# Kernel optimization log

Hardware: AMD Instinct MI355X
Metric: run time of the kernel (lower is better)

Reference implementation:

```python
import jax, jax.numpy as jnp
import numpy as np

B, NQ, D, H, L, P, FFN = 32, 300, 256, 8, 3, 4, 1024
SPATIAL = [(80, 80), (40, 40), (20, 20)]  # static multi-scale feature shapes (640px, strides 8/16/32)
S = sum(h * w for h, w in SPATIAL)  # 8400
HD = D // H


def _ln(x, g, b, eps=1e-5):
    m = jnp.mean(x, -1, keepdims=True)
    v = jnp.mean((x - m) ** 2, -1, keepdims=True)
    return (x - m) * jax.lax.rsqrt(v + eps) * g + b


def _grid_sample(img, grid):
    # img: (N,C,Hh,Ww); grid: (N,Q,Pp,2) in [-1,1]; bilinear, zeros padding, align_corners=False
    N, C, Hh, Ww = img.shape
    x = (grid[..., 0] + 1.0) * (Ww * 0.5) - 0.5
    y = (grid[..., 1] + 1.0) * (Hh * 0.5) - 0.5
    x0 = jnp.floor(x)
    y0 = jnp.floor(y)
    wx1 = x - x0
    wy1 = y - y0
    x0i = x0.astype(jnp.int32)
    y0i = y0.astype(jnp.int32)
    flat = img.reshape(N, C, Hh * Ww)
    Q, Pp = grid.shape[1], grid.shape[2]

    def corner(xi, yi, w):
        valid = (xi >= 0) & (xi < Ww) & (yi >= 0) & (yi < Hh)
        idx = jnp.clip(yi, 0, Hh - 1) * Ww + jnp.clip(xi, 0, Ww - 1)
        v = jnp.take_along_axis(flat, idx.reshape(N, 1, Q * Pp), axis=2).reshape(N, C, Q, Pp)
        return v * (w * valid)[:, None]

    return (corner(x0i, y0i, (1 - wx1) * (1 - wy1))
            + corner(x0i + 1, y0i, wx1 * (1 - wy1))
            + corner(x0i, y0i + 1, (1 - wx1) * wy1)
            + corner(x0i + 1, y0i + 1, wx1 * wy1))


def setup_inputs() -> dict:
    key = jax.random.key(0)
    ks = iter(jax.random.split(key, 32))
    inp = {
        'hidden_states': jax.random.normal(next(ks), (B, NQ, D), jnp.float32),
        'position_embeddings': jax.random.normal(next(ks), (B, NQ, D), jnp.float32),
        'reference_points': jax.random.uniform(next(ks), (B, NQ, 1, 4), jnp.float32, 0.1, 0.9),
        'encoder_hidden_states': jax.random.normal(next(ks), (B, S, D), jnp.float32),
    }
    for name, shape in [('Wq', (D, D)), ('Wk', (D, D)), ('Wv', (D, D)), ('Wo', (D, D)),
                        ('Woff', (D, H * L * P * 2)), ('Waw', (D, H * L * P)),
                        ('Wval', (D, D)), ('Wout', (D, D)), ('W1', (D, FFN)), ('W2', (FFN, D))]:
        inp[name] = jax.random.normal(next(ks), shape, jnp.float32) * 0.02
    for name, dim in [('bq', D), ('bk', D), ('bv', D), ('bo', D), ('boff', H * L * P * 2),
                      ('baw', H * L * P), ('bval', D), ('bout', D), ('b1', FFN), ('b2', D)]:
        inp[name] = jnp.zeros((dim,), jnp.float32)
    for g, bname in [('ln1_g', 'ln1_b'), ('ln2_g', 'ln2_b'), ('ln3_g', 'ln3_b')]:
        inp[g] = jnp.ones((D,), jnp.float32)
        inp[bname] = jnp.zeros((D,), jnp.float32)
    return inp


def reference(hidden_states, position_embeddings, reference_points, encoder_hidden_states,
              Wq, bq, Wk, bk, Wv, bv, Wo, bo, ln1_g, ln1_b,
              Woff, boff, Waw, baw, Wval, bval, Wout, bout, ln2_g, ln2_b,
              W1, b1, W2, b2, ln3_g, ln3_b):
    hs = hidden_states
    # ---- self attention (pos-embedded q/k, raw v) ----
    hp = hs + position_embeddings
    q = ((hp @ Wq + bq) * (HD ** -0.5)).reshape(B, NQ, H, HD)
    k = (hp @ Wk + bk).reshape(B, NQ, H, HD)
    v = (hs @ Wv + bv).reshape(B, NQ, H, HD)
    attn = jax.nn.softmax(jnp.einsum('bqhd,bkhd->bhqk', q, k), axis=-1)
    sa = jnp.einsum('bhqk,bkhd->bqhd', attn, v).reshape(B, NQ, D) @ Wo + bo
    hs = _ln(hs + sa, ln1_g, ln1_b)
    # ---- multi-scale deformable cross attention ----
    hp = hs + position_embeddings
    value = (encoder_hidden_states @ Wval + bval).reshape(B, S, H, HD)
    off = (hp @ Woff + boff).reshape(B, NQ, H, L, P, 2)
    aw = jax.nn.softmax((hp @ Waw + baw).reshape(B, NQ, H, L * P), axis=-1).reshape(B, NQ, H, L, P)
    ref = reference_points  # (B,NQ,1,4) boxes -> 4-coord branch
    loc = ref[:, :, None, :, None, :2] + off / P * ref[:, :, None, :, None, 2:] * 0.5
    grids = (2.0 * loc - 1.0).transpose(0, 2, 1, 3, 4, 5).reshape(B * H, NQ, L, P, 2)
    start = 0
    samples = []
    for lvl, (hh, ww) in enumerate(SPATIAL):
        v_l = value[:, start:start + hh * ww]  # (B,hw,H,HD)
        start += hh * ww
        v_l = v_l.transpose(0, 2, 3, 1).reshape(B * H, HD, hh, ww)
        samples.append(_grid_sample(v_l, grids[:, :, lvl]))  # (B*H,HD,NQ,P)
    sampled = jnp.stack(samples, axis=3).reshape(B * H, HD, NQ, L * P)
    w = aw.transpose(0, 2, 1, 3, 4).reshape(B * H, 1, NQ, L * P)
    ca = (sampled * w).sum(-1).reshape(B, H * HD, NQ).transpose(0, 2, 1) @ Wout + bout
    hs = _ln(hs + ca, ln2_g, ln2_b)
    # ---- FFN ----
    ff = jax.nn.relu(hs @ W1 + b1) @ W2 + b2
    return _ln(hs + ff, ln3_g, ln3_b)
```

## Files before the change

kernel.cpp:

```cpp
#include <hip/hip_runtime.h>
#include <hip/hip_bf16.h>

typedef unsigned int  uint32;
typedef unsigned short ushort16;
typedef __bf16 bfx8 __attribute__((ext_vector_type(8)));
typedef float  f32x4 __attribute__((ext_vector_type(4)));

typedef __attribute__((address_space(1))) const unsigned int gas_u32;
typedef __attribute__((address_space(3))) unsigned int las_u32;

#define B_   32
#define NQ_  300
#define D_   256
#define H_   8
#define HD_  32
#define L_   3
#define P_   4
#define S_   8400
#define FFN_ 1024
#define M1   (B_*NQ_)
#define MV   (B_*S_)
#define NQP  320
#define NQT  19

__device__ inline ushort16 f2bf(float x) {
  uint32 u = __float_as_uint(x);
  uint32 r = u + 0x7fffu + ((u >> 16) & 1u);
  return (ushort16)(r >> 16);
}
__device__ inline float bf2f(ushort16 v) {
  return __uint_as_float(((uint32)v) << 16);
}
__device__ inline uint32 cvtpk(float lo, float hi) {
  uint32 r; asm("v_cvt_pk_bf16_f32 %0, %1, %2" : "=v"(r) : "v"(lo), "v"(hi)); return r;
}

__global__ __launch_bounds__(256) void rt_add(const float* __restrict__ a,
                                              const float* __restrict__ b,
                                              float* __restrict__ o, int n4)
{
  int i = blockIdx.x * 256 + threadIdx.x;
  if (i < n4) {
    float4 x = ((const float4*)a)[i];
    float4 y = ((const float4*)b)[i];
    float4 z; z.x = x.x + y.x; z.y = x.y + y.y; z.z = x.z + y.z; z.w = x.w + y.w;
    ((float4*)o)[i] = z;
  }
}

__global__ __launch_bounds__(256) void rt_wt(const float* __restrict__ W,
                                             ushort16* __restrict__ WT,
                                             int K, int N, int Npad)
{
  __shared__ float t[32][33];
  int n0 = blockIdx.x * 32, k0 = blockIdx.y * 32;
  int c = threadIdx.x & 31, r = threadIdx.x >> 5;
#pragma unroll
  for (int i = 0; i < 4; i++) {
    int kk = k0 + r + i * 8;
    int nn = n0 + c;
    t[r + i * 8][c] = (nn < N) ? W[(size_t)kk * N + nn] : 0.f;
  }
  __syncthreads();
#pragma unroll
  for (int i = 0; i < 4; i++) {
    int nn = n0 + r + i * 8;
    int kk = k0 + c;
    if (nn < Npad) WT[(size_t)nn * K + kk] = f2bf(t[c][r + i * 8]);
  }
}

__global__ __launch_bounds__(256) void rt_wc(const float* __restrict__ W,
                                             ushort16* __restrict__ WC)
{
  int gid = blockIdx.x * 256 + threadIdx.x;
  int c = gid >> 8, n = gid & 255;
  uint4 u;
  uint32 w0 = (uint32)f2bf(W[(c*8+0)*256 + n]) | ((uint32)f2bf(W[(c*8+1)*256 + n]) << 16);
  uint32 w1 = (uint32)f2bf(W[(c*8+2)*256 + n]) | ((uint32)f2bf(W[(c*8+3)*256 + n]) << 16);
  uint32 w2 = (uint32)f2bf(W[(c*8+4)*256 + n]) | ((uint32)f2bf(W[(c*8+5)*256 + n]) << 16);
  uint32 w3 = (uint32)f2bf(W[(c*8+6)*256 + n]) | ((uint32)f2bf(W[(c*8+7)*256 + n]) << 16);
  u.x = w0; u.y = w1; u.z = w2; u.w = w3;
  *(uint4*)&WC[(size_t)c * 2048 + n * 8] = u;
}

__global__ __launch_bounds__(1024, 1) void rt_vgemm(
    const float* __restrict__ A, const ushort16* __restrict__ BC,
    const float* __restrict__ bias, ushort16* __restrict__ Vout)
{
  __shared__ __align__(16) char ldsB[131072];
  const int tid = threadIdx.x;
  const int lane = tid & 63, w = tid >> 6;
  const int l15 = lane & 15, l4 = lane >> 4;
  const int bm = blockIdx.x * 256;
  const int arow = bm + w * 16 + l15;
  const float* Ap = A + (size_t)arow * 256 + l4 * 8;

#pragma unroll
  for (int i = 0; i < 8; ++i)
    __builtin_amdgcn_global_load_lds(
        (gas_u32*)(const void*)((const char*)BC + tid * 16 + i * 16384),
        (las_u32*)(void*)(&ldsB[tid * 16 + i * 16384]), 16, 0, 0);

  f32x4 aA = *(const f32x4*)(Ap +  0);
  f32x4 aB = *(const f32x4*)(Ap +  4);
  f32x4 aC = *(const f32x4*)(Ap + 32);
  f32x4 aD = *(const f32x4*)(Ap + 36);

  f32x4 acc[16];
#pragma unroll
  for (int i = 0; i < 16; ++i) acc[i] = (f32x4){0.f, 0.f, 0.f, 0.f};

  __syncthreads();

#pragma unroll
  for (int tt = 0; tt < 4; ++tt) {
    {
      const int t = 2 * tt;
      uint4 u;
      u.x = cvtpk(aA[0], aA[1]); u.y = cvtpk(aA[2], aA[3]);
      u.z = cvtpk(aB[0], aB[1]); u.w = cvtpk(aB[2], aB[3]);
      bfx8 af = __builtin_bit_cast(bfx8, u);
      if (tt < 3) {
        aA = *(const f32x4*)(Ap + (t + 2) * 32);
        aB = *(const f32x4*)(Ap + (t + 2) * 32 + 4);
      }
      const char* bp = &ldsB[(t * 4 + l4) * 4096 + l15 * 16];
#pragma unroll
      for (int ni = 0; ni < 16; ++ni) {
        bfx8 bg = *(const bfx8*)(const void*)(bp + ni * 256);
        acc[ni] = __builtin_amdgcn_mfma_f32_16x16x32_bf16(af, bg, acc[ni], 0, 0, 0);
      }
    }
    {
      const int t = 2 * tt + 1;
      uint4 u;
      u.x = cvtpk(aC[0], aC[1]); u.y = cvtpk(aC[2], aC[3]);
      u.z = cvtpk(aD[0], aD[1]); u.w = cvtpk(aD[2], aD[3]);
      bfx8 af = __builtin_bit_cast(bfx8, u);
      if (tt < 3) {
        aC = *(const f32x4*)(Ap + (t + 2) * 32);
        aD = *(const f32x4*)(Ap + (t + 2) * 32 + 4);
      }
      const char* bp = &ldsB[(t * 4 + l4) * 4096 + l15 * 16];
#pragma unroll
      for (int ni = 0; ni < 16; ++ni) {
        bfx8 bg = *(const bfx8*)(const void*)(bp + ni * 256);
        acc[ni] = __builtin_amdgcn_mfma_f32_16x16x32_bf16(af, bg, acc[ni], 0, 0, 0);
      }
    }
  }

  const int orow = bm + w * 16 + l4 * 4;
#pragma unroll
  for (int ni = 0; ni < 16; ++ni) {
    int col = ni * 16 + l15;
    float bv = bias[col];
    int hh = col >> 5, hd = col & 31;
#pragma unroll
    for (int r = 0; r < 4; ++r) {
      int row = orow + r;
      int bb = row / S_, s = row - bb * S_;
      Vout[(((size_t)bb * H_ + hh) * S_ + s) * HD_ + hd] = f2bf(acc[ni][r] + bv);
    }
  }
}

#define GBM 128
#define GBN 128
#define GBK 32
#define LDP 40

__global__ __launch_bounds__(256) void rt_mgemm(
    const float* __restrict__ A, const ushort16* __restrict__ BT,
    const float* __restrict__ bias, float* __restrict__ C,
    ushort16* __restrict__ Sc,
    int M, int N, int K, float scale, int mode)
{
  __shared__ __align__(16) ushort16 As[GBM][LDP];
  __shared__ __align__(16) ushort16 Bs[GBN][LDP];
  const int tid  = threadIdx.x;
  const int lane = tid & 63;
  const int w    = tid >> 6;
  const int wr   = (w >> 1) * 64;
  const int wc   = (w & 1) * 64;
  const int bm   = blockIdx.y * GBM;
  const int bn   = blockIdx.x * GBN;
  const int l15  = lane & 15;
  const int l4   = lane >> 4;

  f32x4 acc[4][4];
#pragma unroll
  for (int i = 0; i < 4; i++)
#pragma unroll
    for (int j = 0; j < 4; j++)
      acc[i][j] = (f32x4){0.f, 0.f, 0.f, 0.f};

  const int arow = tid >> 3, akc = tid & 7;
  const int brow = tid >> 2, bkc = tid & 3;

  for (int k0 = 0; k0 < K; k0 += GBK) {
#pragma unroll
    for (int i = 0; i < 4; i++) {
      int row = arow + i * 32;
      f32x4 v = *(const f32x4*)(A + (size_t)(bm + row) * K + k0 + akc * 4);
      uint2 u;
      u.x = (uint32)f2bf(v.x) | ((uint32)f2bf(v.y) << 16);
      u.y = (uint32)f2bf(v.z) | ((uint32)f2bf(v.w) << 16);
      *(uint2*)(&As[row][akc * 4]) = u;
    }
#pragma unroll
    for (int i = 0; i < 2; i++) {
      int row = brow + i * 64;
      uint4 v = *(const uint4*)(BT + (size_t)(bn + row) * K + k0 + bkc * 8);
      *(uint4*)(&Bs[row][bkc * 8]) = v;
    }
    __syncthreads();

    bfx8 af[4], bg[4];
#pragma unroll
    for (int mi = 0; mi < 4; mi++)
      af[mi] = *(const bfx8*)(&As[wr + mi * 16 + l15][l4 * 8]);
#pragma unroll
    for (int ni = 0; ni < 4; ni++)
      bg[ni] = *(const bfx8*)(&Bs[wc + ni * 16 + l15][l4 * 8]);
#pragma unroll
    for (int mi = 0; mi < 4; mi++)
#pragma unroll
      for (int ni = 0; ni < 4; ni++)
        acc[mi][ni] = __builtin_amdgcn_mfma_f32_16x16x32_bf16(af[mi], bg[ni], acc[mi][ni], 0, 0, 0);
    __syncthreads();
  }

#pragma unroll
  for (int mi = 0; mi < 4; mi++) {
#pragma unroll
    for (int ni = 0; ni < 4; ni++) {
      int col = bn + wc + ni * 16 + l15;
      if (col >= N) continue;
      float bv = bias[col];
#pragma unroll
      for (int r = 0; r < 4; r++) {
        int row = bm + wr + mi * 16 + l4 * 4 + r;
        float vv = (acc[mi][ni][r] + bv) * scale;
        if (mode == 1) vv = fmaxf(vv, 0.f);
        if (mode == 2) {
          int bb = row / S_, s = row - bb * S_;
          int hh = col >> 5, hd = col & 31;
          Sc[(((size_t)bb * H_ + hh) * S_ + s) * HD_ + hd] = f2bf(vv);
        } else if (mode == 3) {
          int bb = row / NQ_, q = row - bb * NQ_;
          int hh = col >> 5, hd = col & 31;
          Sc[(((size_t)bb * H_ + hh) * NQP + q) * HD_ + hd] = f2bf(vv);
        } else {
          C[(size_t)row * N + col] = vv;
        }
      }
    }
  }
}

__global__ __launch_bounds__(256) void rt_vtr(const ushort16* __restrict__ vh,
                                              ushort16* __restrict__ vt)
{
  __shared__ ushort16 t[64][33];
  int bh = blockIdx.x;
  const ushort16* src = vh + (size_t)bh * NQP * HD_;
  ushort16* dst = vt + (size_t)bh * HD_ * NQP;
  int tid = threadIdx.x;
  int lrow = tid >> 2, lc8 = (tid & 3) * 8;
  int ohd = tid >> 3, oq8 = (tid & 7) * 8;
  for (int r0 = 0; r0 < NQP; r0 += 64) {
    uint4 v = *(const uint4*)(src + (size_t)(r0 + lrow) * HD_ + lc8);
    ushort16* tp = &t[lrow][lc8];
    tp[0] = (ushort16)(v.x & 0xffff); tp[1] = (ushort16)(v.x >> 16);
    tp[2] = (ushort16)(v.y & 0xffff); tp[3] = (ushort16)(v.y >> 16);
    tp[4] = (ushort16)(v.z & 0xffff); tp[5] = (ushort16)(v.z >> 16);
    tp[6] = (ushort16)(v.w & 0xffff); tp[7] = (ushort16)(v.w >> 16);
    __syncthreads();
    uint4 o;
    o.x = (uint32)t[oq8 + 0][ohd] | ((uint32)t[oq8 + 1][ohd] << 16);
    o.y = (uint32)t[oq8 + 2][ohd] | ((uint32)t[oq8 + 3][ohd] << 16);
    o.z = (uint32)t[oq8 + 4][ohd] | ((uint32)t[oq8 + 5][ohd] << 16);
    o.w = (uint32)t[oq8 + 6][ohd] | ((uint32)t[oq8 + 7][ohd] << 16);
    *(uint4*)(dst + (size_t)ohd * NQP + r0 + oq8) = o;
    __syncthreads();
  }
}

__global__ __launch_bounds__(256) void rt_fattn(
    const ushort16* __restrict__ qh, const ushort16* __restrict__ kh,
    const ushort16* __restrict__ vt, float* __restrict__ O)
{
  int gw  = blockIdx.x * 4 + (threadIdx.x >> 6);
  int bh  = gw / NQT, qt = gw - bh * NQT;
  int b   = bh >> 3, h = bh & 7;
  int lane = threadIdx.x & 63;
  int l15 = lane & 15, l4 = lane >> 4;
  int kb4 = l4 * 4;
  const ushort16* Qb = qh + (size_t)bh * NQP * HD_;
  const ushort16* Kb = kh + (size_t)bh * NQP * HD_;
  const ushort16* Vb = vt + (size_t)bh * HD_ * NQP;
  int q = qt * 16 + l15;

  bfx8 bgQ = *(const bfx8*)(const void*)(Qb + (size_t)q * HD_ + l4 * 8);
  f32x4 o0 = {0.f,0.f,0.f,0.f}, o1 = {0.f,0.f,0.f,0.f};
  float m = -1e30f, ssum = 0.f;

  for (int k0 = 0; k0 < NQP; k0 += 32) {
    bfx8 afk0 = *(const bfx8*)(const void*)(Kb + (size_t)(k0 + l15) * HD_ + l4 * 8);
    bfx8 afk1 = *(const bfx8*)(const void*)(Kb + (size_t)(k0 + 16 + l15) * HD_ + l4 * 8);
    f32x4 z = {0.f,0.f,0.f,0.f};
    f32x4 s0 = __builtin_amdgcn_mfma_f32_16x16x32_bf16(afk0, bgQ, z, 0, 0, 0);
    f32x4 s1 = __builtin_amdgcn_mfma_f32_16x16x32_bf16(afk1, bgQ, z, 0, 0, 0);
    int ka = k0 + kb4, kbb = k0 + 16 + kb4;
#pragma unroll
    for (int r = 0; r < 4; r++) {
      if (ka  + r >= NQ_) s0[r] = -1e30f;
      if (kbb + r >= NQ_) s1[r] = -1e30f;
    }
    float cm = fmaxf(fmaxf(fmaxf(s0[0], s0[1]), fmaxf(s0[2], s0[3])),
                     fmaxf(fmaxf(s1[0], s1[1]), fmaxf(s1[2], s1[3])));
    cm = fmaxf(cm, __shfl_xor(cm, 16));
    cm = fmaxf(cm, __shfl_xor(cm, 32));
    float nm = fmaxf(m, cm);
    float sc = __expf(m - nm);
    m = nm;
    f32x4 p0, p1;
#pragma unroll
    for (int r = 0; r < 4; r++) { p0[r] = __expf(s0[r] - m); p1[r] = __expf(s1[r] - m); }
    float ls = (p0[0]+p0[1]+p0[2]+p0[3]) + (p1[0]+p1[1]+p1[2]+p1[3]);
    ls += __shfl_xor(ls, 16);
    ls += __shfl_xor(ls, 32);
    ssum = ssum * sc + ls;

    uint32 t0w0 = cvtpk(p0[0], p0[1]);
    uint32 t0w1 = cvtpk(p0[2], p0[3]);
    uint32 t1w0 = cvtpk(p1[0], p1[1]);
    uint32 t1w1 = cvtpk(p1[2], p1[3]);
    int srcA = l15 + 32 * (l4 & 1);
    int srcB = srcA + 16;
    uint32 a00 = __shfl((int)t0w0, srcA), a01 = __shfl((int)t0w1, srcA);
    uint32 b00 = __shfl((int)t0w0, srcB), b01 = __shfl((int)t0w1, srcB);
    uint32 a10 = __shfl((int)t1w0, srcA), a11 = __shfl((int)t1w1, srcA);
    uint32 b10 = __shfl((int)t1w0, srcB), b11 = __shfl((int)t1w1, srcB);
    bool hi = (l4 >= 2);
    uint4 pw;
    pw.x = hi ? a10 : a00;
    pw.y = hi ? a11 : a01;
    pw.z = hi ? b10 : b00;
    pw.w = hi ? b11 : b01;
    bfx8 bgP = __builtin_bit_cast(bfx8, pw);

    bfx8 afv0 = *(const bfx8*)(const void*)(Vb + (size_t)l15 * NQP + k0 + l4 * 8);
    bfx8 afv1 = *(const bfx8*)(const void*)(Vb + (size_t)(16 + l15) * NQP + k0 + l4 * 8);
#pragma unroll
    for (int r = 0; r < 4; r++) { o0[r] *= sc; o1[r] *= sc; }
    o0 = __builtin_amdgcn_mfma_f32_16x16x32_bf16(afv0, bgP, o0, 0, 0, 0);
    o1 = __builtin_amdgcn_mfma_f32_16x16x32_bf16(afv1, bgP, o1, 0, 0, 0);
  }

  if (q < NQ_) {
    float inv = 1.f / ssum;
    float* op = O + ((size_t)(b * NQ_ + q)) * D_ + h * HD_ + kb4;
    f32x4 r0, r1;
#pragma unroll
    for (int r = 0; r < 4; r++) { r0[r] = o0[r] * inv; r1[r] = o1[r] * inv; }
    *(f32x4*)op = r0;
    *(f32x4*)(op + 16) = r1;
  }
}

__global__ __launch_bounds__(256) void rt_ln(
    const float* __restrict__ X, const float* __restrict__ R,
    const float* __restrict__ g, const float* __restrict__ be,
    float* __restrict__ O, int rows)
{
  int row = blockIdx.x * 4 + (threadIdx.x >> 6);
  int lane = threadIdx.x & 63;
  if (row >= rows) return;
  size_t base = (size_t)row * D_ + lane * 4;
  float4 x = *(const float4*)(X + base);
  float4 r = *(const float4*)(R + base);
  float v0 = x.x + r.x, v1 = x.y + r.y, v2 = x.z + r.z, v3 = x.w + r.w;
  float s = v0 + v1 + v2 + v3;
  float sq = v0*v0 + v1*v1 + v2*v2 + v3*v3;
#pragma unroll
  for (int o = 32; o >= 1; o >>= 1) { s += __shfl_xor(s, o); sq += __shfl_xor(sq, o); }
  float mean = s * (1.f / D_);
  float var  = sq * (1.f / D_) - mean * mean;
  float inv  = 1.f / sqrtf(var + 1e-5f);
  int c = lane * 4;
  float4 gv = *(const float4*)(g + c);
  float4 bv = *(const float4*)(be + c);
  float4 o4;
  o4.x = (v0 - mean) * inv * gv.x + bv.x;
  o4.y = (v1 - mean) * inv * gv.y + bv.y;
  o4.z = (v2 - mean) * inv * gv.z + bv.z;
  o4.w = (v3 - mean) * inv * gv.w + bv.w;
  *(float4*)(O + base) = o4;
}

__global__ __launch_bounds__(256) void rt_awsm(float* __restrict__ aw, int groups)
{
  int gidx = blockIdx.x * 256 + threadIdx.x;
  if (gidx >= groups) return;
  float* p = aw + (size_t)gidx * 12;
  float e[12]; float m = -1e30f;
#pragma unroll
  for (int i = 0; i < 12; i++) { e[i] = p[i]; m = fmaxf(m, e[i]); }
  float s = 0.f;
#pragma unroll
  for (int i = 0; i < 12; i++) { e[i] = __expf(e[i] - m); s += e[i]; }
  float inv = 1.f / s;
#pragma unroll
  for (int i = 0; i < 12; i++) p[i] = e[i] * inv;
}

__device__ inline void rt_acc8(const ushort16* p, float wgt, float* acc) {
  uint4 v = *(const uint4*)(const void*)p;
  acc[0] += wgt * __uint_as_float(v.x << 16);
  acc[1] += wgt * __uint_as_float(v.x & 0xffff0000u);
  acc[2] += wgt * __uint_as_float(v.y << 16);
  acc[3] += wgt * __uint_as_float(v.y & 0xffff0000u);
  acc[4] += wgt * __uint_as_float(v.z << 16);
  acc[5] += wgt * __uint_as_float(v.z & 0xffff0000u);
  acc[6] += wgt * __uint_as_float(v.w << 16);
  acc[7] += wgt * __uint_as_float(v.w & 0xffff0000u);
}

__global__ __launch_bounds__(256) void rt_deform(
    const ushort16* __restrict__ value,
    const float* __restrict__ off,
    const float* __restrict__ aw,
    const float* __restrict__ ref,
    float* __restrict__ O)
{
  int gid = blockIdx.x * 256 + threadIdx.x;
  int hd0 = (gid & 3) * 8;
  int bqh = gid >> 2;
  int h   = bqh & 7;
  int bq  = bqh >> 3;
  int b   = bq / NQ_;
  const float* rp = ref + (size_t)bq * 4;
  float rx = rp[0], ry = rp[1];
  float rw = rp[2] * 0.125f, rh = rp[3] * 0.125f;
  const float* op = off + (size_t)bqh * 24;
  const float* ap = aw  + (size_t)bqh * 12;
  const ushort16* vb = value + ((size_t)b * H_ + h) * (size_t)S_ * HD_ + hd0;
  float acc[8];
#pragma unroll
  for (int i = 0; i < 8; i++) acc[i] = 0.f;
  const int starts[3] = {0, 6400, 8000};
  const int dims[3]   = {80, 40, 20};
#pragma unroll
  for (int l = 0; l < L_; l++) {
    const int Wl = dims[l];
    const ushort16* vl = vb + (size_t)starts[l] * HD_;
#pragma unroll
    for (int p = 0; p < P_; p++) {
      int ip = l * P_ + p;
      float w = ap[ip];
      float x = (rx + op[ip*2+0] * rw) * Wl - 0.5f;
      float y = (ry + op[ip*2+1] * rh) * Wl - 0.5f;
      float x0f = floorf(x), y0f = floorf(y);
      int   x0 = (int)x0f,  y0 = (int)y0f;
      float wx1 = x - x0f, wy1 = y - y0f;
      float wx0 = 1.f - wx1, wy0 = 1.f - wy1;
      bool xok0 = (x0 >= 0) & (x0 < Wl), xok1 = (x0+1 >= 0) & (x0+1 < Wl);
      bool yok0 = (y0 >= 0) & (y0 < Wl), yok1 = (y0+1 >= 0) & (y0+1 < Wl);
      const ushort16* r0p = vl + (size_t)(y0 * Wl) * HD_;
      const ushort16* r1p = r0p + (size_t)Wl * HD_;
      if (xok0 & yok0) rt_acc8(r0p + (size_t)x0 * HD_,     w * wx0 * wy0, acc);
      if (xok1 & yok0) rt_acc8(r0p + (size_t)(x0+1) * HD_, w * wx1 * wy0, acc);
      if (xok0 & yok1) rt_acc8(r1p + (size_t)x0 * HD_,     w * wx0 * wy1, acc);
      if (xok1 & yok1) rt_acc8(r1p + (size_t)(x0+1) * HD_, w * wx1 * wy1, acc);
    }
  }
  float* outp = O + (size_t)bq * D_ + h * HD_ + hd0;
  float4 a0, a1;
  a0.x = acc[0]; a0.y = acc[1]; a0.z = acc[2]; a0.w = acc[3];
  a1.x = acc[4]; a1.y = acc[5]; a1.z = acc[6]; a1.w = acc[7];
  *(float4*)outp = a0;
  *(float4*)(outp + 4) = a1;
}

extern "C" void kernel_launch(void* const* d_in, const int* in_sizes, int n_in,
                              void* d_out, int out_size, void* d_ws, size_t ws_size,
                              hipStream_t stream)
{
  const float* hs   = (const float*)d_in[0];
  const float* pos  = (const float*)d_in[1];
  const float* ref  = (const float*)d_in[2];
  const float* ehs  = (const float*)d_in[3];
  const float* Wq   = (const float*)d_in[4];
  const float* Wk   = (const float*)d_in[5];
  const float* Wv   = (const float*)d_in[6];
  const float* Wo   = (const float*)d_in[7];
  const float* Woff = (const float*)d_in[8];
  const float* Waw  = (const float*)d_in[9];
  const float* Wval = (const float*)d_in[10];
  const float* Wout = (const float*)d_in[11];
  const float* W1   = (const float*)d_in[12];
  const float* W2   = (const float*)d_in[13];
  const float* bq   = (const float*)d_in[14];
  const float* bk   = (const float*)d_in[15];
  const float* bvv  = (const float*)d_in[16];
  const float* bo   = (const float*)d_in[17];
  const float* boff = (const float*)d_in[18];
  const float* baw  = (const float*)d_in[19];
  const float* bval = (const float*)d_in[20];
  const float* bout = (const float*)d_in[21];
  const float* b1   = (const float*)d_in[22];
  const float* b2   = (const float*)d_in[23];
  const float* ln1g = (const float*)d_in[24];
  const float* ln1b = (const float*)d_in[25];
  const float* ln2g = (const float*)d_in[26];
  const float* ln2b = (const float*)d_in[27];
  const float* ln3g = (const float*)d_in[28];
  const float* ln3b = (const float*)d_in[29];
  float* out = (float*)d_out;

  float* ws = (float*)d_ws;
  ushort16* value = (ushort16*)ws;
  float* hp   = ws + 34406400;
  float* t0   = ws + 36864000;
  float* t1   = ws + 39321600;
  float* hs1  = ws + 41779200;
  float* hs2  = ws + 44236800;
  float* offb = ws + 46694400;
  float* awb  = ws + 48537600;
  float* ffn1 = ws + 49459200;
  ushort16* qh = (ushort16*)(ws + 59289600);
  ushort16* kh = (ushort16*)(ws + 60600320);
  ushort16* vh = (ushort16*)(ws + 61911040);
  ushort16* vt = (ushort16*)(ws + 63221760);
  ushort16* wbase = (ushort16*)(ws + 64532480);
  ushort16* WqT   = wbase;
  ushort16* WkT   = WqT   + 65536;
  ushort16* WvT   = WkT   + 65536;
  ushort16* WoT   = WvT   + 65536;
  ushort16* WoffT = WoT   + 65536;
  ushort16* WawT  = WoffT + 65536;
  ushort16* WvalC = WawT  + 32768;
  ushort16* WoutT = WvalC + 65536;
  ushort16* W1T   = WoutT + 65536;
  ushort16* W2T   = W1T   + 262144;

  const float qscale = 0.17677669529663687f;

  rt_wt<<<dim3(8, 8),  256, 0, stream>>>(Wq,   WqT,   256, 256, 256);
  rt_wt<<<dim3(8, 8),  256, 0, stream>>>(Wk,   WkT,   256, 256, 256);
  rt_wt<<<dim3(8, 8),  256, 0, stream>>>(Wv,   WvT,   256, 256, 256);
  rt_wt<<<dim3(8, 8),  256, 0, stream>>>(Wo,   WoT,   256, 256, 256);
  rt_wt<<<dim3(8, 8),  256, 0, stream>>>(Woff, WoffT, 256, 192, 256);
  rt_wt<<<dim3(4, 8),  256, 0, stream>>>(Waw,  WawT,  256,  96, 128);
  rt_wc<<<dim3(32),    256, 0, stream>>>(Wval, WvalC);
  rt_wt<<<dim3(8, 8),  256, 0, stream>>>(Wout, WoutT, 256, 256, 256);
  rt_wt<<<dim3(32, 8), 256, 0, stream>>>(W1,   W1T,   256, 1024, 1024);
  rt_wt<<<dim3(8, 32), 256, 0, stream>>>(W2,   W2T,   1024, 256, 256);

  rt_vgemm<<<dim3(MV/256), 1024, 0, stream>>>(ehs, WvalC, bval, value);

  rt_add<<<dim3(M1*D_/4/256), 256, 0, stream>>>(hs, pos, hp, M1*D_/4);
  rt_mgemm<<<dim3(2, M1/GBM), 256, 0, stream>>>(hp, WqT, bq,  nullptr, qh, M1, D_, D_, qscale, 3);
  rt_mgemm<<<dim3(2, M1/GBM), 256, 0, stream>>>(hp, WkT, bk,  nullptr, kh, M1, D_, D_, 1.f, 3);
  rt_mgemm<<<dim3(2, M1/GBM), 256, 0, stream>>>(hs, WvT, bvv, nullptr, vh, M1, D_, D_, 1.f, 3);
  rt_vtr<<<dim3(B_*H_), 256, 0, stream>>>(vh, vt);
  rt_fattn<<<dim3(B_*H_*NQT/4), 256, 0, stream>>>(qh, kh, vt, t0);
  rt_mgemm<<<dim3(2, M1/GBM), 256, 0, stream>>>(t0, WoT, bo, t1, nullptr, M1, D_, D_, 1.f, 0);
  rt_ln<<<dim3(M1/4), 256, 0, stream>>>(hs, t1, ln1g, ln1b, hs1, M1);
  rt_add<<<dim3(M1*D_/4/256), 256, 0, stream>>>(hs1, pos, hp, M1*D_/4);
  rt_mgemm<<<dim3(2, M1/GBM), 256, 0, stream>>>(hp, WoffT, boff, offb, nullptr, M1, 192, D_, 1.f, 0);
  rt_mgemm<<<dim3(1, M1/GBM), 256, 0, stream>>>(hp, WawT,  baw,  awb,  nullptr, M1,  96, D_, 1.f, 0);
  rt_awsm<<<dim3(B_*NQ_*H_/256), 256, 0, stream>>>(awb, B_*NQ_*H_);
  rt_deform<<<dim3(M1*H_*4/256), 256, 0, stream>>>(value, offb, awb, ref, t0);
  rt_mgemm<<<dim3(2, M1/GBM), 256, 0, stream>>>(t0, WoutT, bout, t1, nullptr, M1, D_, D_, 1.f, 0);
  rt_ln<<<dim3(M1/4), 256, 0, stream>>>(hs1, t1, ln2g, ln2b, hs2, M1);
  rt_mgemm<<<dim3(8, M1/GBM), 256, 0, stream>>>(hs2, W1T, b1, ffn1, nullptr, M1, FFN_, D_, 1.f, 1);
  rt_mgemm<<<dim3(2, M1/GBM), 256, 0, stream>>>(ffn1, W2T, b2, t1, nullptr, M1, D_, FFN_, 1.f, 0);
  rt_ln<<<dim3(M1/4), 256, 0, stream>>>(hs2, t1, ln3g, ln3b, out, M1);
}
```

Before: 466.8 us.

## Batch weight prep, persist value GEMM, fuse QK/offset-aw GEMMs and softmax into deform

Ten weight-transpose launches become one rt_wprep kernel, which also folds the query scale into Wq and bq and concatenates the biases. The value-projection GEMM becomes a persistent 256-block kernel that loads the weight into LDS once per block. It swaps the MFMA operand order so each lane stores four consecutive head-dim elements as packed bf16. The Q and K projections merge into one 512-wide GEMM with a split scatter, and the offset and attention-weight projections merge into one 288-wide GEMM. The aw softmax moves inside the deform kernel, cutting launches and intermediate round trips at the cost of recomputing the softmax per head-dim lane group.

```diff
diff --git a/kernel.cpp b/kernel.cpp
--- a/kernel.cpp
+++ b/kernel.cpp
@@ -28,9 +28,6 @@
   uint32 r = u + 0x7fffu + ((u >> 16) & 1u);
   return (ushort16)(r >> 16);
 }
-__device__ inline float bf2f(ushort16 v) {
-  return __uint_as_float(((uint32)v) << 16);
-}
 __device__ inline uint32 cvtpk(float lo, float hi) {
   uint32 r; asm("v_cvt_pk_bf16_f32 %0, %1, %2" : "=v"(r) : "v"(lo), "v"(hi)); return r;
 }
@@ -48,40 +45,60 @@
   }
 }
 
-__global__ __launch_bounds__(256) void rt_wt(const float* __restrict__ W,
-                                             ushort16* __restrict__ WT,
-                                             int K, int N, int Npad)
+struct WPrep {
+  const float* src[9];
+  ushort16*    dst[9];
+  int K[9], N[9], Npad[9], tileEnd[9];
+  float scale[9];
+  const float* wval; ushort16* wvalc;
+  const float* bqs;  const float* bks;  float* bqk;
+  const float* boffs; const float* baws; float* boffaw;
+};
+
+__global__ __launch_bounds__(256) void rt_wprep(WPrep a)
 {
   __shared__ float t[32][33];
-  int n0 = blockIdx.x * 32, k0 = blockIdx.y * 32;
-  int c = threadIdx.x & 31, r = threadIdx.x >> 5;
-#pragma unroll
-  for (int i = 0; i < 4; i++) {
-    int kk = k0 + r + i * 8;
-    int nn = n0 + c;
-    t[r + i * 8][c] = (nn < N) ? W[(size_t)kk * N + nn] : 0.f;
-  }
-  __syncthreads();
-#pragma unroll
-  for (int i = 0; i < 4; i++) {
-    int nn = n0 + r + i * 8;
-    int kk = k0 + c;
-    if (nn < Npad) WT[(size_t)nn * K + kk] = f2bf(t[c][r + i * 8]);
-  }
-}
-
-__global__ __launch_bounds__(256) void rt_wc(const float* __restrict__ W,
-                                             ushort16* __restrict__ WC)
-{
-  int gid = blockIdx.x * 256 + threadIdx.x;
-  int c = gid >> 8, n = gid & 255;
-  uint4 u;
-  uint32 w0 = (uint32)f2bf(W[(c*8+0)*256 + n]) | ((uint32)f2bf(W[(c*8+1)*256 + n]) << 16);
-  uint32 w1 = (uint32)f2bf(W[(c*8+2)*256 + n]) | ((uint32)f2bf(W[(c*8+3)*256 + n]) << 16);
-  uint32 w2 = (uint32)f2bf(W[(c*8+4)*256 + n]) | ((uint32)f2bf(W[(c*8+5)*256 + n]) << 16);
-  uint32 w3 = (uint32)f2bf(W[(c*8+6)*256 + n]) | ((uint32)f2bf(W[(c*8+7)*256 + n]) << 16);
-  u.x = w0; u.y = w1; u.z = w2; u.w = w3;
-  *(uint4*)&WC[(size_t)c * 2048 + n * 8] = u;
+  int blk = blockIdx.x;
+  if (blk < 904) {
+    int wi = 0;
+    while (blk >= a.tileEnd[wi]) wi++;
+    int base = wi ? a.tileEnd[wi - 1] : 0;
+    int idx = blk - base;
+    int K = a.K[wi], N = a.N[wi];
+    int ntx = a.Npad[wi] / 32;
+    int n0 = (idx % ntx) * 32, k0 = (idx / ntx) * 32;
+    float sc = a.scale[wi];
+    const float* W = a.src[wi];
+    ushort16* WT = a.dst[wi];
+    int c = threadIdx.x & 31, r = threadIdx.x >> 5;
+#pragma unroll
+    for (int i = 0; i < 4; i++) {
+      int nn = n0 + c;
+      t[r + i * 8][c] = (nn < N) ? W[(size_t)(k0 + r + i * 8) * N + nn] : 0.f;
+    }
+    __syncthreads();
+#pragma unroll
+    for (int i = 0; i < 4; i++)
+      WT[(size_t)(n0 + r + i * 8) * K + k0 + c] = f2bf(t[c][r + i * 8] * sc);
+  } else if (blk < 936) {
+    int gid = (blk - 904) * 256 + threadIdx.x;
+    int c = gid >> 8, n = gid & 255;
+    const float* W = a.wval;
+    uint4 u;
+    u.x = (uint32)f2bf(W[(c*8+0)*256 + n]) | ((uint32)f2bf(W[(c*8+1)*256 + n]) << 16);
+    u.y = (uint32)f2bf(W[(c*8+2)*256 + n]) | ((uint32)f2bf(W[(c*8+3)*256 + n]) << 16);
+    u.z = (uint32)f2bf(W[(c*8+4)*256 + n]) | ((uint32)f2bf(W[(c*8+5)*256 + n]) << 16);
+    u.w = (uint32)f2bf(W[(c*8+6)*256 + n]) | ((uint32)f2bf(W[(c*8+7)*256 + n]) << 16);
+    *(uint4*)&a.wvalc[(size_t)c * 2048 + n * 8] = u;
+  } else if (blk == 936) {
+    a.bqk[threadIdx.x] = a.bqs[threadIdx.x] * a.scale[0];
+  } else if (blk == 937) {
+    a.bqk[256 + threadIdx.x] = a.bks[threadIdx.x];
+  } else if (blk == 938) {
+    if (threadIdx.x < 192) a.boffaw[threadIdx.x] = a.boffs[threadIdx.x];
+  } else {
+    if (threadIdx.x < 96) a.boffaw[192 + threadIdx.x] = a.baws[threadIdx.x];
+  }
 }
 
 __global__ __launch_bounds__(1024, 1) void rt_vgemm(
@@ -92,76 +109,72 @@
   const int tid = threadIdx.x;
   const int lane = tid & 63, w = tid >> 6;
   const int l15 = lane & 15, l4 = lane >> 4;
-  const int bm = blockIdx.x * 256;
-  const int arow = bm + w * 16 + l15;
-  const float* Ap = A + (size_t)arow * 256 + l4 * 8;
 
 #pragma unroll
   for (int i = 0; i < 8; ++i)
     __builtin_amdgcn_global_load_lds(
         (gas_u32*)(const void*)((const char*)BC + tid * 16 + i * 16384),
         (las_u32*)(void*)(&ldsB[tid * 16 + i * 16384]), 16, 0, 0);
-
-  f32x4 aA = *(const f32x4*)(Ap +  0);
-  f32x4 aB = *(const f32x4*)(Ap +  4);
-  f32x4 aC = *(const f32x4*)(Ap + 32);
-  f32x4 aD = *(const f32x4*)(Ap + 36);
-
-  f32x4 acc[16];
-#pragma unroll
-  for (int i = 0; i < 16; ++i) acc[i] = (f32x4){0.f, 0.f, 0.f, 0.f};
-
   __syncthreads();
 
-#pragma unroll
-  for (int tt = 0; tt < 4; ++tt) {
-    {
-      const int t = 2 * tt;
-      uint4 u;
-      u.x = cvtpk(aA[0], aA[1]); u.y = cvtpk(aA[2], aA[3]);
-      u.z = cvtpk(aB[0], aB[1]); u.w = cvtpk(aB[2], aB[3]);
-      bfx8 af = __builtin_bit_cast(bfx8, u);
-      if (tt < 3) {
-        aA = *(const f32x4*)(Ap + (t + 2) * 32);
-        aB = *(const f32x4*)(Ap + (t + 2) * 32 + 4);
+  const int wrow = w * 16 + l15;
+  for (int t = blockIdx.x; t < MV / 256; t += 256) {
+    const float* Ap = A + ((size_t)t * 256 + wrow) * 256 + l4 * 8;
+    f32x4 aA = *(const f32x4*)(Ap);
+    f32x4 aB = *(const f32x4*)(Ap + 4);
+    f32x4 aC = *(const f32x4*)(Ap + 32);
+    f32x4 aD = *(const f32x4*)(Ap + 36);
+    f32x4 acc[16];
+#pragma unroll
+    for (int i = 0; i < 16; ++i) acc[i] = (f32x4){0.f, 0.f, 0.f, 0.f};
+
+#pragma unroll
+    for (int tt = 0; tt < 4; ++tt) {
+      {
+        uint4 u;
+        u.x = cvtpk(aA[0], aA[1]); u.y = cvtpk(aA[2], aA[3]);
+        u.z = cvtpk(aB[0], aB[1]); u.w = cvtpk(aB[2], aB[3]);
+        bfx8 af = __builtin_bit_cast(bfx8, u);
+        if (tt < 3) {
+          aA = *(const f32x4*)(Ap + (2 * tt + 2) * 32);
+          aB = *(const f32x4*)(Ap + (2 * tt + 2) * 32 + 4);
+        }
+        const char* bp = &ldsB[(2 * tt * 4 + l4) * 4096 + l15 * 16];
+#pragma unroll
+        for (int ni = 0; ni < 16; ++ni) {
+          bfx8 bg = *(const bfx8*)(const void*)(bp + ni * 256);
+          acc[ni] = __builtin_amdgcn_mfma_f32_16x16x32_bf16(bg, af, acc[ni], 0, 0, 0);
+        }
       }
-      const char* bp = &ldsB[(t * 4 + l4) * 4096 + l15 * 16];
-#pragma unroll
-      for (int ni = 0; ni < 16; ++ni) {
-        bfx8 bg = *(const bfx8*)(const void*)(bp + ni * 256);
-        acc[ni] = __builtin_amdgcn_mfma_f32_16x16x32_bf16(af, bg, acc[ni], 0, 0, 0);
+      {
+        uint4 u;
+        u.x = cvtpk(aC[0], aC[1]); u.y = cvtpk(aC[2], aC[3]);
+        u.z = cvtpk(aD[0], aD[1]); u.w = cvtpk(aD[2], aD[3]);
+        bfx8 af = __builtin_bit_cast(bfx8, u);
+        if (tt < 3) {
+          aC = *(const f32x4*)(Ap + (2 * tt + 3) * 32);
+          aD = *(const f32x4*)(Ap + (2 * tt + 3) * 32 + 4);
+        }
+        const char* bp = &ldsB[((2 * tt + 1) * 4 + l4) * 4096 + l15 * 16];
+#pragma unroll
+        for (int ni = 0; ni < 16; ++ni) {
+          bfx8 bg = *(const bfx8*)(const void*)(bp + ni * 256);
+          acc[ni] = __builtin_amdgcn_mfma_f32_16x16x32_bf16(bg, af, acc[ni], 0, 0, 0);
+        }
       }
     }
-    {
-      const int t = 2 * tt + 1;
-      uint4 u;
-      u.x = cvtpk(aC[0], aC[1]); u.y = cvtpk(aC[2], aC[3]);
-      u.z = cvtpk(aD[0], aD[1]); u.w = cvtpk(aD[2], aD[3]);
-      bfx8 af = __builtin_bit_cast(bfx8, u);
-      if (tt < 3) {
-        aC = *(const f32x4*)(Ap + (t + 2) * 32);
-        aD = *(const f32x4*)(Ap + (t + 2) * 32 + 4);
-      }
-      const char* bp = &ldsB[(t * 4 + l4) * 4096 + l15 * 16];
-#pragma unroll
-      for (int ni = 0; ni < 16; ++ni) {
-        bfx8 bg = *(const bfx8*)(const void*)(bp + ni * 256);
-        acc[ni] = __builtin_amdgcn_mfma_f32_16x16x32_bf16(af, bg, acc[ni], 0, 0, 0);
-      }
-    }
-  }
-
-  const int orow = bm + w * 16 + l4 * 4;
-#pragma unroll
-  for (int ni = 0; ni < 16; ++ni) {
-    int col = ni * 16 + l15;
-    float bv = bias[col];
-    int hh = col >> 5, hd = col & 31;
-#pragma unroll
-    for (int r = 0; r < 4; ++r) {
-      int row = orow + r;
-      int bb = row / S_, s = row - bb * S_;
-      Vout[(((size_t)bb * H_ + hh) * S_ + s) * HD_ + hd] = f2bf(acc[ni][r] + bv);
+    int row = t * 256 + wrow;
+    int bb = row / S_, s = row - bb * S_;
+    ushort16* vb = Vout + (((size_t)bb * H_) * S_ + s) * HD_;
+#pragma unroll
+    for (int ni = 0; ni < 16; ++ni) {
+      int col = ni * 16 + l4 * 4;
+      f32x4 bv = *(const f32x4*)(bias + col);
+      int hh = col >> 5, hd = col & 31;
+      uint2 st;
+      st.x = cvtpk(acc[ni][0] + bv[0], acc[ni][1] + bv[1]);
+      st.y = cvtpk(acc[ni][2] + bv[2], acc[ni][3] + bv[3]);
+      *(uint2*)(vb + (size_t)hh * S_ * HD_ + hd) = st;
     }
   }
 }
@@ -174,7 +187,7 @@
 __global__ __launch_bounds__(256) void rt_mgemm(
     const float* __restrict__ A, const ushort16* __restrict__ BT,
     const float* __restrict__ bias, float* __restrict__ C,
-    ushort16* __restrict__ Sc,
+    ushort16* __restrict__ Sc, ushort16* __restrict__ Sc2,
     int M, int N, int K, float scale, int mode)
 {
   __shared__ __align__(16) ushort16 As[GBM][LDP];
@@ -205,8 +218,8 @@
       int row = arow + i * 32;
       f32x4 v = *(const f32x4*)(A + (size_t)(bm + row) * K + k0 + akc * 4);
       uint2 u;
-      u.x = (uint32)f2bf(v.x) | ((uint32)f2bf(v.y) << 16);
-      u.y = (uint32)f2bf(v.z) | ((uint32)f2bf(v.w) << 16);
+      u.x = cvtpk(v.x, v.y);
+      u.y = cvtpk(v.z, v.w);
       *(uint2*)(&As[row][akc * 4]) = u;
     }
 #pragma unroll
@@ -244,14 +257,15 @@
         int row = bm + wr + mi * 16 + l4 * 4 + r;
         float vv = (acc[mi][ni][r] + bv) * scale;
         if (mode == 1) vv = fmaxf(vv, 0.f);
-        if (mode == 2) {
-          int bb = row / S_, s = row - bb * S_;
-          int hh = col >> 5, hd = col & 31;
-          Sc[(((size_t)bb * H_ + hh) * S_ + s) * HD_ + hd] = f2bf(vv);
-        } else if (mode == 3) {
+        if (mode == 3) {
           int bb = row / NQ_, q = row - bb * NQ_;
           int hh = col >> 5, hd = col & 31;
           Sc[(((size_t)bb * H_ + hh) * NQP + q) * HD_ + hd] = f2bf(vv);
+        } else if (mode == 4) {
+          int bb = row / NQ_, q = row - bb * NQ_;
+          int hh = col >> 5, hd = col & 31;
+          ushort16* d = (hh < 8) ? Sc : Sc2;
+          d[(((size_t)bb * H_ + (hh & 7)) * NQP + q) * HD_ + hd] = f2bf(vv);
         } else {
           C[(size_t)row * N + col] = vv;
         }
@@ -401,22 +415,6 @@
   *(float4*)(O + base) = o4;
 }
 
-__global__ __launch_bounds__(256) void rt_awsm(float* __restrict__ aw, int groups)
-{
-  int gidx = blockIdx.x * 256 + threadIdx.x;
-  if (gidx >= groups) return;
-  float* p = aw + (size_t)gidx * 12;
-  float e[12]; float m = -1e30f;
-#pragma unroll
-  for (int i = 0; i < 12; i++) { e[i] = p[i]; m = fmaxf(m, e[i]); }
-  float s = 0.f;
-#pragma unroll
-  for (int i = 0; i < 12; i++) { e[i] = __expf(e[i] - m); s += e[i]; }
-  float inv = 1.f / s;
-#pragma unroll
-  for (int i = 0; i < 12; i++) p[i] = e[i] * inv;
-}
-
 __device__ inline void rt_acc8(const ushort16* p, float wgt, float* acc) {
   uint4 v = *(const uint4*)(const void*)p;
   acc[0] += wgt * __uint_as_float(v.x << 16);
@@ -431,8 +429,7 @@
 
 __global__ __launch_bounds__(256) void rt_deform(
     const ushort16* __restrict__ value,
-    const float* __restrict__ off,
-    const float* __restrict__ aw,
+    const float* __restrict__ offaw,
     const float* __restrict__ ref,
     float* __restrict__ O)
 {
@@ -445,8 +442,16 @@
   const float* rp = ref + (size_t)bq * 4;
   float rx = rp[0], ry = rp[1];
   float rw = rp[2] * 0.125f, rh = rp[3] * 0.125f;
-  const float* op = off + (size_t)bqh * 24;
-  const float* ap = aw  + (size_t)bqh * 12;
+  const float* op = offaw + (size_t)bq * 288 + h * 24;
+  const float* ap = offaw + (size_t)bq * 288 + 192 + h * 12;
+  float e[12]; float mx = -1e30f;
+#pragma unroll
+  for (int i = 0; i < 12; i++) { e[i] = ap[i]; mx = fmaxf(mx, e[i]); }
+  float ssum = 0.f;
+#pragma unroll
+  for (int i = 0; i < 12; i++) { e[i] = __expf(e[i] - mx); ssum += e[i]; }
+  float sinv = 1.f / ssum;
+
   const ushort16* vb = value + ((size_t)b * H_ + h) * (size_t)S_ * HD_ + hd0;
   float acc[8];
 #pragma unroll
@@ -460,7 +465,7 @@
 #pragma unroll
     for (int p = 0; p < P_; p++) {
       int ip = l * P_ + p;
-      float w = ap[ip];
+      float wgt = e[ip] * sinv;
       float x = (rx + op[ip*2+0] * rw) * Wl - 0.5f;
       float y = (ry + op[ip*2+1] * rh) * Wl - 0.5f;
       float x0f = floorf(x), y0f = floorf(y);
@@ -471,10 +476,10 @@
       bool yok0 = (y0 >= 0) & (y0 < Wl), yok1 = (y0+1 >= 0) & (y0+1 < Wl);
       const ushort16* r0p = vl + (size_t)(y0 * Wl) * HD_;
       const ushort16* r1p = r0p + (size_t)Wl * HD_;
-      if (xok0 & yok0) rt_acc8(r0p + (size_t)x0 * HD_,     w * wx0 * wy0, acc);
-      if (xok1 & yok0) rt_acc8(r0p + (size_t)(x0+1) * HD_, w * wx1 * wy0, acc);
-      if (xok0 & yok1) rt_acc8(r1p + (size_t)x0 * HD_,     w * wx0 * wy1, acc);
-      if (xok1 & yok1) rt_acc8(r1p + (size_t)(x0+1) * HD_, w * wx1 * wy1, acc);
+      if (xok0 & yok0) rt_acc8(r0p + (size_t)x0 * HD_,     wgt * wx0 * wy0, acc);
+      if (xok1 & yok0) rt_acc8(r0p + (size_t)(x0+1) * HD_, wgt * wx1 * wy0, acc);
+      if (xok0 & yok1) rt_acc8(r1p + (size_t)x0 * HD_,     wgt * wx0 * wy1, acc);
+      if (xok1 & yok1) rt_acc8(r1p + (size_t)(x0+1) * HD_, wgt * wx1 * wy1, acc);
     }
   }
   float* outp = O + (size_t)bq * D_ + h * HD_ + hd0;
@@ -523,61 +528,64 @@
 
   float* ws = (float*)d_ws;
   ushort16* value = (ushort16*)ws;
-  float* hp   = ws + 34406400;
-  float* t0   = ws + 36864000;
-  float* t1   = ws + 39321600;
-  float* hs1  = ws + 41779200;
-  float* hs2  = ws + 44236800;
-  float* offb = ws + 46694400;
-  float* awb  = ws + 48537600;
-  float* ffn1 = ws + 49459200;
+  float* hp     = ws + 34406400;
+  float* t0     = ws + 36864000;
+  float* t1     = ws + 39321600;
+  float* hs1    = ws + 41779200;
+  float* hs2    = ws + 44236800;
+  float* offawb = ws + 46694400;
+  float* ffn1   = ws + 49459200;
   ushort16* qh = (ushort16*)(ws + 59289600);
   ushort16* kh = (ushort16*)(ws + 60600320);
   ushort16* vh = (ushort16*)(ws + 61911040);
   ushort16* vt = (ushort16*)(ws + 63221760);
-  ushort16* wbase = (ushort16*)(ws + 64532480);
-  ushort16* WqT   = wbase;
-  ushort16* WkT   = WqT   + 65536;
-  ushort16* WvT   = WkT   + 65536;
-  ushort16* WoT   = WvT   + 65536;
-  ushort16* WoffT = WoT   + 65536;
-  ushort16* WawT  = WoffT + 65536;
-  ushort16* WvalC = WawT  + 32768;
-  ushort16* WoutT = WvalC + 65536;
-  ushort16* W1T   = WoutT + 65536;
-  ushort16* W2T   = W1T   + 262144;
+  ushort16* wbase  = (ushort16*)(ws + 64532480);
+  ushort16* WqkT   = wbase;
+  ushort16* WvT    = WqkT   + 131072;
+  ushort16* WoT    = WvT    + 65536;
+  ushort16* WoffawT= WoT    + 65536;
+  ushort16* WoutT  = WoffawT+ 98304;
+  ushort16* W1T    = WoutT  + 65536;
+  ushort16* W2T    = W1T    + 262144;
+  ushort16* WvalC  = W2T    + 262144;
+  float* bqk    = (float*)(WvalC + 65536);
+  float* boffaw = bqk + 512;
 
   const float qscale = 0.17677669529663687f;
 
-  rt_wt<<<dim3(8, 8),  256, 0, stream>>>(Wq,   WqT,   256, 256, 256);
-  rt_wt<<<dim3(8, 8),  256, 0, stream>>>(Wk,   WkT,   256, 256, 256);
-  rt_wt<<<dim3(8, 8),  256, 0, stream>>>(Wv,   WvT,   256, 256, 256);
-  rt_wt<<<dim3(8, 8),  256, 0, stream>>>(Wo,   WoT,   256, 256, 256);
-  rt_wt<<<dim3(8, 8),  256, 0, stream>>>(Woff, WoffT, 256, 192, 256);
-  rt_wt<<<dim3(4, 8),  256, 0, stream>>>(Waw,  WawT,  256,  96, 128);
-  rt_wc<<<dim3(32),    256, 0, stream>>>(Wval, WvalC);
-  rt_wt<<<dim3(8, 8),  256, 0, stream>>>(Wout, WoutT, 256, 256, 256);
-  rt_wt<<<dim3(32, 8), 256, 0, stream>>>(W1,   W1T,   256, 1024, 1024);
-  rt_wt<<<dim3(8, 32), 256, 0, stream>>>(W2,   W2T,   1024, 256, 256);
-
-  rt_vgemm<<<dim3(MV/256), 1024, 0, stream>>>(ehs, WvalC, bval, value);
+  WPrep a;
+  a.src[0]=Wq;   a.dst[0]=WqkT;            a.K[0]=256;  a.N[0]=256;  a.Npad[0]=256; a.scale[0]=qscale;
+  a.src[1]=Wk;   a.dst[1]=WqkT+65536;      a.K[1]=256;  a.N[1]=256;  a.Npad[1]=256; a.scale[1]=1.f;
+  a.src[2]=Wv;   a.dst[2]=WvT;             a.K[2]=256;  a.N[2]=256;  a.Npad[2]=256; a.scale[2]=1.f;
+  a.src[3]=Wo;   a.dst[3]=WoT;             a.K[3]=256;  a.N[3]=256;  a.Npad[3]=256; a.scale[3]=1.f;
+  a.src[4]=Woff; a.dst[4]=WoffawT;         a.K[4]=256;  a.N[4]=192;  a.Npad[4]=192; a.scale[4]=1.f;
+  a.src[5]=Waw;  a.dst[5]=WoffawT+49152;   a.K[5]=256;  a.N[5]=96;   a.Npad[5]=96;  a.scale[5]=1.f;
+  a.src[6]=Wout; a.dst[6]=WoutT;           a.K[6]=256;  a.N[6]=256;  a.Npad[6]=256; a.scale[6]=1.f;
+  a.src[7]=W1;   a.dst[7]=W1T;             a.K[7]=256;  a.N[7]=1024; a.Npad[7]=1024;a.scale[7]=1.f;
+  a.src[8]=W2;   a.dst[8]=W2T;             a.K[8]=1024; a.N[8]=256;  a.Npad[8]=256; a.scale[8]=1.f;
+  int cum = 0;
+  int tiles[9] = {64, 64, 64, 64, 48, 24, 64, 256, 256};
+  for (int i = 0; i < 9; i++) { cum += tiles[i]; a.tileEnd[i] = cum; }
+  a.wval = Wval; a.wvalc = WvalC;
+  a.bqs = bq; a.bks = bk; a.bqk = bqk;
+  a.boffs = boff; a.baws = baw; a.boffaw = boffaw;
+  rt_wprep<<<dim3(940), 256, 0, stream>>>(a);
+
+  rt_vgemm<<<dim3(256), 1024, 0, stream>>>(ehs, WvalC, bval, value);
 
   rt_add<<<dim3(M1*D_/4/256), 256, 0, stream>>>(hs, pos, hp, M1*D_/4);
-  rt_mgemm<<<dim3(2, M1/GBM), 256, 0, stream>>>(hp, WqT, bq,  nullptr, qh, M1, D_, D_, qscale, 3);
-  rt_mgemm<<<dim3(2, M1/GBM), 256, 0, stream>>>(hp, WkT, bk,  nullptr, kh, M1, D_, D_, 1.f, 3);
-  rt_mgemm<<<dim3(2, M1/GBM), 256, 0, stream>>>(hs, WvT, bvv, nullptr, vh, M1, D_, D_, 1.f, 3);
+  rt_mgemm<<<dim3(4, M1/GBM), 256, 0, stream>>>(hp, WqkT, bqk, nullptr, qh, kh, M1, 512, D_, 1.f, 4);
+  rt_mgemm<<<dim3(2, M1/GBM), 256, 0, stream>>>(hs, WvT, bvv, nullptr, vh, vh, M1, D_, D_, 1.f, 3);
   rt_vtr<<<dim3(B_*H_), 256, 0, stream>>>(vh, vt);
   rt_fattn<<<dim3(B_*H_*NQT/4), 256, 0, stream>>>(qh, kh, vt, t0);
-  rt_mgemm<<<dim3(2, M1/GBM), 256, 0, stream>>>(t0, WoT, bo, t1, nullptr, M1, D_, D_, 1.f, 0);
+  rt_mgemm<<<dim3(2, M1/GBM), 256, 0, stream>>>(t0, WoT, bo, t1, nullptr, nullptr, M1, D_, D_, 1.f, 0);
   rt_ln<<<dim3(M1/4), 256, 0, stream>>>(hs, t1, ln1g, ln1b, hs1, M1);
   rt_add<<<dim3(M1*D_/4/256), 256, 0, stream>>>(hs1, pos, hp, M1*D_/4);
-  rt_mgemm<<<dim3(2, M1/GBM), 256, 0, stream>>>(hp, WoffT, boff, offb, nullptr, M1, 192, D_, 1.f, 0);
-  rt_mgemm<<<dim3(1, M1/GBM), 256, 0, stream>>>(hp, WawT,  baw,  awb,  nullptr, M1,  96, D_, 1.f, 0);
-  rt_awsm<<<dim3(B_*NQ_*H_/256), 256, 0, stream>>>(awb, B_*NQ_*H_);
-  rt_deform<<<dim3(M1*H_*4/256), 256, 0, stream>>>(value, offb, awb, ref, t0);
-  rt_mgemm<<<dim3(2, M1/GBM), 256, 0, stream>>>(t0, WoutT, bout, t1, nullptr, M1, D_, D_, 1.f, 0);
+  rt_mgemm<<<dim3(3, M1/GBM), 256, 0, stream>>>(hp, WoffawT, boffaw, offawb, nullptr, nullptr, M1, 288, D_, 1.f, 0);
+  rt_deform<<<dim3(M1*H_*4/256), 256, 0, stream>>>(value, offawb, ref, t0);
+  rt_mgemm<<<dim3(2, M1/GBM), 256, 0, stream>>>(t0, WoutT, bout, t1, nullptr, nullptr, M1, D_, D_, 1.f, 0);
   rt_ln<<<dim3(M1/4), 256, 0, stream>>>(hs1, t1, ln2g, ln2b, hs2, M1);
-  rt_mgemm<<<dim3(8, M1/GBM), 256, 0, stream>>>(hs2, W1T, b1, ffn1, nullptr, M1, FFN_, D_, 1.f, 1);
-  rt_mgemm<<<dim3(2, M1/GBM), 256, 0, stream>>>(ffn1, W2T, b2, t1, nullptr, M1, D_, FFN_, 1.f, 0);
+  rt_mgemm<<<dim3(8, M1/GBM), 256, 0, stream>>>(hs2, W1T, b1, ffn1, nullptr, nullptr, M1, FFN_, D_, 1.f, 1);
+  rt_mgemm<<<dim3(2, M1/GBM), 256, 0, stream>>>(ffn1, W2T, b2, t1, nullptr, nullptr, M1, D_, FFN_, 1.f, 0);
   rt_ln<<<dim3(M1/4), 256, 0, stream>>>(hs2, t1, ln3g, ln3b, out, M1);
 }
```

New measurement: 387.5 us. -17.0%, faster.
